# Performance work log

Measured on AMD Instinct MI355X. Metric: run time of the kernel, lower is better.

The kernel has to match this reference:

```python
import jax, jax.numpy as jnp
import numpy as np

V = 17  # number of skeleton joints (hard-coded in the torch module)
NUM_SUBSET = 3

def _dam_mask():
    # Reproduces the Python masking loops: zero block [12:17,12:17] and rows/cols {3,6,7,9,10}
    m = np.ones((V, V), np.float32)
    m[12:17, 12:17] = 0.0
    for j in (3, 6, 7, 9, 10):
        m[j, :] = 0.0
        m[:, j] = 0.0
    return jnp.asarray(m)

def setup_inputs() -> dict:
    key = jax.random.key(0)
    ks = jax.random.split(key, 8)
    N, Cin, Cout, T, G = 64, 64, 64, 256, 8
    return {
        "x": jax.random.normal(ks[0], (N, Cin, T, V), jnp.float32),
        "A_base": jax.random.uniform(ks[1], (NUM_SUBSET, V, V), jnp.float32),  # fixed adjacency buffer
        "DA": 0.01 * jax.random.normal(ks[2], (NUM_SUBSET, G, V, V), jnp.float32),   # DecoupleA param
        "DAM": 0.01 * jax.random.normal(ks[3], (NUM_SUBSET, G, V, V), jnp.float32),  # DecoupleAM param (masked, detached)
        "conv_w": jax.random.normal(ks[4], (NUM_SUBSET * Cout, Cin), jnp.float32) * (2.0 / Cin) ** 0.5,  # 1x1 conv
        "conv_b": jnp.zeros((NUM_SUBSET * Cout,), jnp.float32),
        "se_w": jax.random.normal(ks[5], (3,), jnp.float32) * 0.5,  # conv2_1: Conv1d(1,1,k=3,pad=1,no bias)
        "bn_gamma": jnp.full((Cout,), 1e-6, jnp.float32),  # bn_init(bn, 1e-6)
        "bn_beta": jnp.zeros((Cout,), jnp.float32),
    }

def reference(x, A_base, DA, DAM, conv_w, conv_b, se_w, bn_gamma, bn_beta):
    G = DA.shape[1]
    Cout = bn_gamma.shape[0]
    N, Cin, T, _ = x.shape
    # --- adjacency assembly: A (buffer, broadcast over groups) + DecoupleA + masked DecoupleAM ---
    A = A_base[:, None] + DA + DAM * _dam_mask()              # [3, G, V, V]
    # torch .repeat(1, out//groups, 1, 1) tiles along channel axis; + 0.04 from A_final loop
    A_final = jnp.tile(A, (1, Cout // G, 1, 1)) + 0.04        # [3, Cout, V, V]
    # --- 1x1 conv C_in -> 3*C_out ---
    m = jnp.einsum('nctv,kc->nktv', x, conv_w) + conv_b[None, :, None, None]
    m = m.reshape(N, NUM_SUBSET, Cout, T, V)
    # --- grouped adjacency aggregation (A_final has no batch dependence) ---
    m = jnp.einsum('nkctv,kcvw->nctw', m, A_final)            # [N, Cout, T, V]
    # --- SE-style channel attention: global avg pool -> Conv1d(k=3) over channels -> sigmoid gate ---
    p = m.mean(axis=(2, 3))                                   # [N, Cout]
    pp = jnp.pad(p, ((0, 0), (1, 1)))
    g = se_w[0] * pp[:, :-2] + se_w[1] * pp[:, 1:-1] + se_w[2] * pp[:, 2:]
    q = m + m * jax.nn.sigmoid(g)[:, :, None, None]
    # --- BatchNorm2d (training mode: batch stats over N,T,V) ---
    mu = q.mean(axis=(0, 2, 3), keepdims=True)
    var = q.var(axis=(0, 2, 3), keepdims=True)
    q = bn_gamma[None, :, None, None] * (q - mu) * jax.lax.rsqrt(var + 1e-5) + bn_beta[None, :, None, None]
    # --- residual (down == identity since in_channels == out_channels) and ReLU ---
    return jax.nn.relu(q + x)
```

## Files before the change

### kernel.cpp

```cpp
#include <hip/hip_runtime.h>
#include <math.h>

#define NN 64
#define CIN 64
#define COUT 64
#define TT 256
#define VV 17
#define NSUB 3
#define GG 8

#define WS_MB 0
#define WS_WBF 12288
#define WS_PSUM 18432
#define WS_SSQ 22528
#define WS_ACOEF 0
#define WS_BCOEF 4096

typedef short bh8 __attribute__((ext_vector_type(8)));
typedef float f32x4 __attribute__((ext_vector_type(4)));
typedef float f32x16 __attribute__((ext_vector_type(16)));
typedef unsigned short u16t;

__device__ __forceinline__ unsigned bf16r(float f) {
    unsigned u = __builtin_bit_cast(unsigned, f);
    return (u + 0x7fffu + ((u >> 16) & 1u)) >> 16;
}
__device__ __forceinline__ float bf2f(unsigned us) {
    return __builtin_bit_cast(float, us << 16);
}

__device__ __forceinline__ float mfull(const float* Ab, const float* DA, const float* DAM,
                                       int s, int g, int v, int w) {
    const unsigned bad = (1u << 3) | (1u << 6) | (1u << 7) | (1u << 9) | (1u << 10);
    float mask = ((v >= 12 && w >= 12) || ((bad >> v) & 1) || ((bad >> w) & 1)) ? 0.f : 1.f;
    int src = ((s * GG + g) * VV + v) * VV + w;
    return Ab[(s * VV + v) * VV + w] + DA[src] + DAM[src] * mask + 0.04f;
}

__global__ void gcn_prep(const float* __restrict__ Ab, const float* __restrict__ DA,
                         const float* __restrict__ DAM, const float* __restrict__ convw,
                         float* __restrict__ ws) {
    int t0 = blockIdx.x * 256 + threadIdx.x;
    int stride = gridDim.x * 256;
    u16t* wbf = (u16t*)(ws + WS_WBF);
    for (int i = t0; i < 192 * 64; i += stride) wbf[i] = (u16t)bf16r(convw[i]);
    u16t* mb = (u16t*)(ws + WS_MB);
    for (int i = t0; i < NSUB * GG * 32 * 32; i += stride) {
        int k = i & 31, w = (i >> 5) & 31, g = (i >> 10) & 7, s = i >> 13;
        u16t val = 0;
        if (w < VV && k < VV) val = (u16t)bf16r(mfull(Ab, DA, DAM, s, g, k, w));
        mb[i] = val;
    }
    for (int i = t0; i < 8192; i += stride) ws[WS_PSUM + i] = 0.f;
}

__global__ __launch_bounds__(512, 2) void gcn_pass1(const float* __restrict__ x,
                                                    const float* __restrict__ convb,
                                                    const float* __restrict__ ws,
                                                    float* __restrict__ out,
                                                    float* __restrict__ psum,
                                                    float* __restrict__ ssq) {
    __shared__ u16t xsT[272 * 72];
    __shared__ u16t Wl[192 * 72];
    __shared__ u16t mt[64 * 648];

    const int tid = threadIdx.x;
    const int wave = tid >> 6;
    const int l = tid & 63;
    const int c16 = l & 15;
    const int q4 = (l >> 4) & 3;
    const int c32 = l & 31;
    const int hi = l >> 5;
    const int n = blockIdx.x >> 2;

    const u16t* mbg = (const u16t*)(ws + WS_MB);
    const u16t* wbfg = (const u16t*)(ws + WS_WBF);

    for (int j = tid; j < 192 * 32; j += 512) {
        int row = j >> 5, c2 = j & 31;
        ((unsigned*)Wl)[row * 36 + c2] = ((const unsigned*)wbfg)[j];
    }
    for (int j = tid; j < (64 * 648) / 2; j += 512) ((unsigned*)mt)[j] = 0u;

    bh8 Badj[3], Badj2[3];
#pragma unroll
    for (int s = 0; s < 3; ++s) {
        const u16t* mrow = &mbg[((s * 8 + wave) * 32 + c32) * 32 + 8 * hi];
        Badj[s] = *(const bh8*)mrow;
        Badj2[s] = *(const bh8*)(mrow + 16);
    }
    const int cfs[3] = {wave, wave + 8, 16};

    float acc1[8], acc2[8];
#pragma unroll
    for (int j = 0; j < 8; ++j) { acc1[j] = 0.f; acc2[j] = 0.f; }

    __syncthreads();

    for (int k4 = 0; k4 < 4; ++k4) {
        const int tt = 4 * (blockIdx.x & 3) + k4;

        const float* xb = x + (size_t)n * 64 * 4352 + tt * 272;
#pragma unroll
        for (int k = 0; k < 4; ++k) {
            int cp = wave + 8 * k;
            const float* r0 = xb + (2 * cp) * 4352;
            const float* r1 = r0 + 4352;
#pragma unroll
            for (int cc = 0; cc < 5; ++cc) {
                int col = cc * 64 + l;
                if (col < 272) {
                    unsigned p = bf16r(r0[col]) | (bf16r(r1[col]) << 16);
                    ((unsigned*)xsT)[col * 36 + cp] = p;
                }
            }
        }
        __syncthreads();

        bh8 Bc[3][2];
#pragma unroll
        for (int cfi = 0; cfi < 3; ++cfi)
#pragma unroll
            for (int ks = 0; ks < 2; ++ks)
                Bc[cfi][ks] = *(const bh8*)&xsT[(16 * cfs[cfi] + c16) * 72 + 32 * ks + 8 * q4];

        f32x16 D2[4];
#pragma unroll
        for (int p = 0; p < 4; ++p) D2[p] = 0;

#pragma unroll
        for (int s = 0; s < 3; ++s) {
            f32x4 Dc[4][3];
#pragma unroll
            for (int rf = 0; rf < 4; ++rf) {
                f32x4 bias = *(const f32x4*)(convb + s * 64 + 16 * rf + 4 * q4);
#pragma unroll
                for (int cfi = 0; cfi < 3; ++cfi) Dc[rf][cfi] = bias;
            }
#pragma unroll
            for (int rf = 0; rf < 4; ++rf)
#pragma unroll
                for (int ks = 0; ks < 2; ++ks) {
                    bh8 A = *(const bh8*)&Wl[(s * 64 + 16 * rf + c16) * 72 + 32 * ks + 8 * q4];
                    Dc[rf][0] = __builtin_amdgcn_mfma_f32_16x16x32_bf16(A, Bc[0][ks], Dc[rf][0], 0, 0, 0);
                    Dc[rf][1] = __builtin_amdgcn_mfma_f32_16x16x32_bf16(A, Bc[1][ks], Dc[rf][1], 0, 0, 0);
                    if (wave == rf)
                        Dc[rf][2] = __builtin_amdgcn_mfma_f32_16x16x32_bf16(A, Bc[2][ks], Dc[rf][2], 0, 0, 0);
                }
            if (s > 0) __syncthreads();
#pragma unroll
            for (int rf = 0; rf < 4; ++rf)
#pragma unroll
                for (int cfi = 0; cfi < 3; ++cfi) {
                    if (cfi == 2 && wave != rf) continue;
                    int col = 16 * cfs[cfi] + c16;
                    int t = (col * 241) >> 12;
                    int v = col - 17 * t;
                    int base = (16 * rf + 4 * q4) * 648 + t * 40 + v;
#pragma unroll
                    for (int i = 0; i < 4; ++i)
                        mt[base + i * 648] = (u16t)bf16r(Dc[rf][cfi][i]);
                }
            __syncthreads();

#pragma unroll
            for (int p = 0; p < 4; ++p) {
                int coA = wave + 8 * (2 * p + (c32 >> 4));
                int base = coA * 648 + c16 * 40 + 8 * hi;
                bh8 a0 = *(const bh8*)&mt[base];
                bh8 a1 = *(const bh8*)&mt[base + 16];
                D2[p] = __builtin_amdgcn_mfma_f32_32x32x16_bf16(a0, Badj[s], D2[p], 0, 0, 0);
                D2[p] = __builtin_amdgcn_mfma_f32_32x32x16_bf16(a1, Badj2[s], D2[p], 0, 0, 0);
            }
        }

        u16t* stg = xsT;
#pragma unroll
        for (int p = 0; p < 4; ++p)
#pragma unroll
            for (int reg = 0; reg < 16; ++reg) {
                int row = (reg & 3) + 8 * (reg >> 2) + 4 * hi;
                int cosel = row >> 4;
                int t = row & 15;
                int co = wave + 8 * (2 * p + cosel);
                float val = D2[p][reg];
                if (c32 < 17) stg[co * 272 + t * 17 + c32] = (u16t)bf16r(val);
                if (cosel == 0) { acc1[2 * p] += val; acc2[2 * p] += val * val; }
                else            { acc1[2 * p + 1] += val; acc2[2 * p + 1] += val * val; }
            }
        __syncthreads();

        float* ob = out + ((size_t)n * 64) * 4352 + tt * 272;
#pragma unroll
        for (int it = 0; it < 9; ++it) {
            int c = tid + 512 * it;
            if (c < 4352) {
                int co = c / 68;
                int pos = (c - co * 68) * 4;
                uint2 u = *(const uint2*)&stg[co * 272 + pos];
                float4 v;
                v.x = bf2f(u.x & 0xffffu);
                v.y = bf2f(u.x >> 16);
                v.z = bf2f(u.y & 0xffffu);
                v.w = bf2f(u.y >> 16);
                *(float4*)(ob + co * 4352 + pos) = v;
            }
        }
        __syncthreads();
    }

#pragma unroll
    for (int j = 0; j < 8; ++j) {
        float s1 = acc1[j], s2 = acc2[j];
#pragma unroll
        for (int m = 1; m < 64; m <<= 1) {
            s1 += __shfl_xor(s1, m);
            s2 += __shfl_xor(s2, m);
        }
        if (l == 0) {
            atomicAdd(&psum[n * 64 + wave + 8 * j], s1);
            atomicAdd(&ssq[n * 64 + wave + 8 * j], s2);
        }
    }
}

__global__ void gcn_stats(const float* __restrict__ se_w, const float* __restrict__ gamma,
                          const float* __restrict__ beta, float* __restrict__ ws) {
    __shared__ float ps[4096], sc[4096], q2s[4096];
    __shared__ float mu_s[64], inv_s[64];
    int tid = threadIdx.x;
    const float* psum = ws + WS_PSUM;
    const float* ssq = ws + WS_SSQ;
    float* acoef = ws + WS_ACOEF;
    float* bcoef = ws + WS_BCOEF;
    for (int i = tid; i < 4096; i += 256) ps[i] = psum[i] * (1.f / (TT * VV));
    __syncthreads();
    float w0 = se_w[0], w1 = se_w[1], w2 = se_w[2];
    for (int i = tid; i < 4096; i += 256) {
        int c = i & 63;
        float pm = (c > 0) ? ps[i - 1] : 0.f;
        float pp = (c < 63) ? ps[i + 1] : 0.f;
        float gg = w0 * pm + w1 * ps[i] + w2 * pp;
        float s = 1.f + 1.f / (1.f + expf(-gg));
        sc[i] = s;
        q2s[i] = s * s * ssq[i];
    }
    __syncthreads();
    if (tid < 64) {
        float mu = 0.f, e2 = 0.f;
        for (int nn = 0; nn < 64; ++nn) {
            mu += sc[nn * 64 + tid] * ps[nn * 64 + tid];
            e2 += q2s[nn * 64 + tid];
        }
        mu *= (1.f / 64.f);
        e2 *= (1.f / (64.f * TT * VV));
        float var = e2 - mu * mu;
        mu_s[tid] = mu;
        inv_s[tid] = rsqrtf(var + 1e-5f);
    }
    __syncthreads();
    for (int i = tid; i < 4096; i += 256) {
        int c = i & 63;
        float gin = gamma[c] * inv_s[c];
        acoef[i] = gin * sc[i];
        bcoef[i] = beta[c] - gin * mu_s[c];
    }
}

__global__ __launch_bounds__(256) void gcn_final(const float* __restrict__ x,
                                                 const float* __restrict__ ws,
                                                 float* __restrict__ out) {
    const float* acoef = ws + WS_ACOEF;
    const float* bcoef = ws + WS_BCOEF;
    int i = blockIdx.x * 256 + threadIdx.x;
    const int total4 = (NN * COUT * TT * VV) / 4;
    if (i >= total4) return;
    int nc = i / ((TT * VV) / 4);
    float a = acoef[nc], b = bcoef[nc];
    float4 m = ((const float4*)out)[i];
    float4 xx = ((const float4*)x)[i];
    float4 r;
    r.x = fmaxf(fmaf(a, m.x, b) + xx.x, 0.f);
    r.y = fmaxf(fmaf(a, m.y, b) + xx.y, 0.f);
    r.z = fmaxf(fmaf(a, m.z, b) + xx.z, 0.f);
    r.w = fmaxf(fmaf(a, m.w, b) + xx.w, 0.f);
    ((float4*)out)[i] = r;
}

extern "C" void kernel_launch(void* const* d_in, const int* in_sizes, int n_in,
                              void* d_out, int out_size, void* d_ws, size_t ws_size,
                              hipStream_t stream) {
    const float* x = (const float*)d_in[0];
    const float* Ab = (const float*)d_in[1];
    const float* DA = (const float*)d_in[2];
    const float* DAM = (const float*)d_in[3];
    const float* convw = (const float*)d_in[4];
    const float* convb = (const float*)d_in[5];
    const float* sew = (const float*)d_in[6];
    const float* gamma = (const float*)d_in[7];
    const float* beta = (const float*)d_in[8];
    float* out = (float*)d_out;
    float* ws = (float*)d_ws;

    gcn_prep<<<16, 256, 0, stream>>>(Ab, DA, DAM, convw, ws);
    gcn_pass1<<<256, 512, 0, stream>>>(x, convb, ws, out, ws + WS_PSUM, ws + WS_SSQ);
    gcn_stats<<<1, 256, 0, stream>>>(sew, gamma, beta, ws);
    const int total4 = (NN * COUT * TT * VV) / 4;
    gcn_final<<<(total4 + 255) / 256, 256, 0, stream>>>(x, ws, out);
}
```

Before: 117.4 us.

## Halve pass1 tile size, store intermediate as bf16, raise occupancy

Pass1 now processes 8 time steps per tile (136 columns) with 512 blocks instead of 256, shrinks shared memory so four blocks can be resident per CU, and loads x as 8-channel packed vectors. When workspace is large enough, the intermediate pre-BN activation is written to a bf16 buffer in workspace instead of fp32 into the output, and a new final kernel reads it back. This halves the intermediate write and read traffic, and the extra workspace requirement is handled by falling back to the fp32 path.

```diff
diff --git a/kernel.cpp b/kernel.cpp
--- a/kernel.cpp
+++ b/kernel.cpp
@@ -15,6 +15,8 @@
 #define WS_SSQ 22528
 #define WS_ACOEF 0
 #define WS_BCOEF 4096
+#define M2BF_BYTE_OFF 131072ull
+#define M2BF_NEED (M2BF_BYTE_OFF + 2ull * 64 * 64 * 256 * 17)
 
 typedef short bh8 __attribute__((ext_vector_type(8)));
 typedef float f32x4 __attribute__((ext_vector_type(4)));
@@ -54,119 +56,131 @@
     for (int i = t0; i < 8192; i += stride) ws[WS_PSUM + i] = 0.f;
 }
 
-__global__ __launch_bounds__(512, 2) void gcn_pass1(const float* __restrict__ x,
+template <int BFOUT>
+__global__ __launch_bounds__(512, 4) void gcn_pass1(const float* __restrict__ x,
                                                     const float* __restrict__ convb,
                                                     const float* __restrict__ ws,
                                                     float* __restrict__ out,
+                                                    u16t* __restrict__ m2b,
                                                     float* __restrict__ psum,
                                                     float* __restrict__ ssq) {
-    __shared__ u16t xsT[272 * 72];
-    __shared__ u16t Wl[192 * 72];
-    __shared__ u16t mt[64 * 648];
+    __shared__ __align__(16) unsigned char smem[73984];
+    u16t* xsT = (u16t*)smem;
+    u16t* Wl = (u16t*)(smem + 20736);
+    u16t* mt = (u16t*)(smem + 48384);
 
     const int tid = threadIdx.x;
-    const int wave = tid >> 6;
+    const int wv = tid >> 6;
     const int l = tid & 63;
     const int c16 = l & 15;
     const int q4 = (l >> 4) & 3;
     const int c32 = l & 31;
     const int hi = l >> 5;
-    const int n = blockIdx.x >> 2;
-
-    const u16t* mbg = (const u16t*)(ws + WS_MB);
-    const u16t* wbfg = (const u16t*)(ws + WS_WBF);
-
-    for (int j = tid; j < 192 * 32; j += 512) {
-        int row = j >> 5, c2 = j & 31;
-        ((unsigned*)Wl)[row * 36 + c2] = ((const unsigned*)wbfg)[j];
-    }
-    for (int j = tid; j < (64 * 648) / 2; j += 512) ((unsigned*)mt)[j] = 0u;
-
+    const int n = blockIdx.x >> 3;
+
+    {
+        const unsigned* wsrc = (const unsigned*)(ws + WS_WBF);
+        unsigned* wd = (unsigned*)Wl;
+        for (int j = tid; j < 192 * 32; j += 512) wd[(j >> 5) * 36 + (j & 31)] = wsrc[j];
+        unsigned* mz = (unsigned*)mt;
+        for (int j = tid; j < 6400; j += 512) mz[j] = 0u;
+    }
+
+    const u16t* mb16 = (const u16t*)(ws + WS_MB);
     bh8 Badj[3], Badj2[3];
 #pragma unroll
     for (int s = 0; s < 3; ++s) {
-        const u16t* mrow = &mbg[((s * 8 + wave) * 32 + c32) * 32 + 8 * hi];
+        const u16t* mrow = &mb16[((s * 8 + wv) * 32 + c32) * 32 + 8 * hi];
         Badj[s] = *(const bh8*)mrow;
         Badj2[s] = *(const bh8*)(mrow + 16);
     }
-    const int cfs[3] = {wave, wave + 8, 16};
 
     float acc1[8], acc2[8];
 #pragma unroll
     for (int j = 0; j < 8; ++j) { acc1[j] = 0.f; acc2[j] = 0.f; }
 
-    __syncthreads();
-
     for (int k4 = 0; k4 < 4; ++k4) {
-        const int tt = 4 * (blockIdx.x & 3) + k4;
-
-        const float* xb = x + (size_t)n * 64 * 4352 + tt * 272;
-#pragma unroll
-        for (int k = 0; k < 4; ++k) {
-            int cp = wave + 8 * k;
-            const float* r0 = xb + (2 * cp) * 4352;
-            const float* r1 = r0 + 4352;
-#pragma unroll
-            for (int cc = 0; cc < 5; ++cc) {
-                int col = cc * 64 + l;
-                if (col < 272) {
-                    unsigned p = bf16r(r0[col]) | (bf16r(r1[col]) << 16);
-                    ((unsigned*)xsT)[col * 36 + cp] = p;
-                }
-            }
+        const int tt = (blockIdx.x & 7) * 4 + k4;
+
+        const float* xb = x + (size_t)n * 64 * 4352 + tt * 136;
+        for (int task = tid; task < 136 * 8; task += 512) {
+            int oct = task / 136;
+            int col = task - 136 * oct;
+            const float* src = xb + (8 * oct) * 4352 + col;
+            float r0 = src[0], r1 = src[4352], r2 = src[2 * 4352], r3 = src[3 * 4352];
+            float r4 = src[4 * 4352], r5 = src[5 * 4352], r6 = src[6 * 4352], r7 = src[7 * 4352];
+            uint4 pk;
+            pk.x = bf16r(r0) | (bf16r(r1) << 16);
+            pk.y = bf16r(r2) | (bf16r(r3) << 16);
+            pk.z = bf16r(r4) | (bf16r(r5) << 16);
+            pk.w = bf16r(r6) | (bf16r(r7) << 16);
+            *(uint4*)&((unsigned*)xsT)[col * 36 + oct * 4] = pk;
         }
         __syncthreads();
 
-        bh8 Bc[3][2];
-#pragma unroll
-        for (int cfi = 0; cfi < 3; ++cfi)
+        bh8 Bc[2], Bc8[2];
+#pragma unroll
+        for (int ks = 0; ks < 2; ++ks)
+            Bc[ks] = *(const bh8*)&xsT[(16 * wv + c16) * 72 + 32 * ks + 8 * q4];
+        if (wv < 4) {
 #pragma unroll
             for (int ks = 0; ks < 2; ++ks)
-                Bc[cfi][ks] = *(const bh8*)&xsT[(16 * cfs[cfi] + c16) * 72 + 32 * ks + 8 * q4];
-
-        f32x16 D2[4];
-#pragma unroll
-        for (int p = 0; p < 4; ++p) D2[p] = 0;
+                Bc8[ks] = *(const bh8*)&xsT[(128 + c16) * 72 + 32 * ks + 8 * q4];
+        }
+
+        f32x16 D2[2];
+        D2[0] = 0; D2[1] = 0;
 
 #pragma unroll
         for (int s = 0; s < 3; ++s) {
-            f32x4 Dc[4][3];
-#pragma unroll
-            for (int rf = 0; rf < 4; ++rf) {
-                f32x4 bias = *(const f32x4*)(convb + s * 64 + 16 * rf + 4 * q4);
-#pragma unroll
-                for (int cfi = 0; cfi < 3; ++cfi) Dc[rf][cfi] = bias;
-            }
+            f32x4 Dc[4], Dc8;
 #pragma unroll
             for (int rf = 0; rf < 4; ++rf)
+                Dc[rf] = *(const f32x4*)(convb + s * 64 + 16 * rf + 4 * q4);
+            if (wv < 4) Dc8 = *(const f32x4*)(convb + s * 64 + 16 * wv + 4 * q4);
+#pragma unroll
+            for (int ks = 0; ks < 2; ++ks)
+#pragma unroll
+                for (int rf = 0; rf < 4; ++rf) {
+                    bh8 A = *(const bh8*)&Wl[(s * 64 + 16 * rf + c16) * 72 + 32 * ks + 8 * q4];
+                    Dc[rf] = __builtin_amdgcn_mfma_f32_16x16x32_bf16(A, Bc[ks], Dc[rf], 0, 0, 0);
+                }
+            if (wv < 4) {
 #pragma unroll
                 for (int ks = 0; ks < 2; ++ks) {
-                    bh8 A = *(const bh8*)&Wl[(s * 64 + 16 * rf + c16) * 72 + 32 * ks + 8 * q4];
-                    Dc[rf][0] = __builtin_amdgcn_mfma_f32_16x16x32_bf16(A, Bc[0][ks], Dc[rf][0], 0, 0, 0);
-                    Dc[rf][1] = __builtin_amdgcn_mfma_f32_16x16x32_bf16(A, Bc[1][ks], Dc[rf][1], 0, 0, 0);
-                    if (wave == rf)
-                        Dc[rf][2] = __builtin_amdgcn_mfma_f32_16x16x32_bf16(A, Bc[2][ks], Dc[rf][2], 0, 0, 0);
-                }
+                    bh8 A = *(const bh8*)&Wl[(s * 64 + 16 * wv + c16) * 72 + 32 * ks + 8 * q4];
+                    Dc8 = __builtin_amdgcn_mfma_f32_16x16x32_bf16(A, Bc8[ks], Dc8, 0, 0, 0);
+                }
+            }
+
             if (s > 0) __syncthreads();
-#pragma unroll
-            for (int rf = 0; rf < 4; ++rf)
-#pragma unroll
-                for (int cfi = 0; cfi < 3; ++cfi) {
-                    if (cfi == 2 && wave != rf) continue;
-                    int col = 16 * cfs[cfi] + c16;
-                    int t = (col * 241) >> 12;
-                    int v = col - 17 * t;
-                    int base = (16 * rf + 4 * q4) * 648 + t * 40 + v;
+            {
+                int col = 16 * wv + c16;
+                int t = (col * 241) >> 12;
+                int v = col - 17 * t;
+                int off = t * 24 + v;
+#pragma unroll
+                for (int rf = 0; rf < 4; ++rf) {
+                    int co0 = 16 * rf + 4 * q4;
 #pragma unroll
                     for (int i = 0; i < 4; ++i)
-                        mt[base + i * 648] = (u16t)bf16r(Dc[rf][cfi][i]);
-                }
+                        mt[(co0 + i) * 200 + off] = (u16t)bf16r(Dc[rf][i]);
+                }
+                if (wv < 4 && c16 < 8) {
+                    int v8 = (128 + c16) - 119;
+                    int off8 = 7 * 24 + v8;
+                    int co0 = 16 * wv + 4 * q4;
+#pragma unroll
+                    for (int i = 0; i < 4; ++i)
+                        mt[(co0 + i) * 200 + off8] = (u16t)bf16r(Dc8[i]);
+                }
+            }
             __syncthreads();
 
 #pragma unroll
-            for (int p = 0; p < 4; ++p) {
-                int coA = wave + 8 * (2 * p + (c32 >> 4));
-                int base = coA * 648 + c16 * 40 + 8 * hi;
+            for (int p = 0; p < 2; ++p) {
+                int co = wv + 8 * ((c32 >> 3) + 4 * p);
+                int base = co * 200 + (c32 & 7) * 24 + 8 * hi;
                 bh8 a0 = *(const bh8*)&mt[base];
                 bh8 a1 = *(const bh8*)&mt[base + 16];
                 D2[p] = __builtin_amdgcn_mfma_f32_32x32x16_bf16(a0, Badj[s], D2[p], 0, 0, 0);
@@ -176,34 +190,48 @@
 
         u16t* stg = xsT;
 #pragma unroll
-        for (int p = 0; p < 4; ++p)
+        for (int p = 0; p < 2; ++p)
 #pragma unroll
             for (int reg = 0; reg < 16; ++reg) {
                 int row = (reg & 3) + 8 * (reg >> 2) + 4 * hi;
-                int cosel = row >> 4;
-                int t = row & 15;
-                int co = wave + 8 * (2 * p + cosel);
+                int cosel = row >> 3;
+                int t = row & 7;
+                int co = wv + 8 * (cosel + 4 * p);
                 float val = D2[p][reg];
-                if (c32 < 17) stg[co * 272 + t * 17 + c32] = (u16t)bf16r(val);
-                if (cosel == 0) { acc1[2 * p] += val; acc2[2 * p] += val * val; }
-                else            { acc1[2 * p + 1] += val; acc2[2 * p + 1] += val * val; }
+                if (c32 < 17) stg[co * 140 + t * 17 + c32] = (u16t)bf16r(val);
+                int j = cosel + 4 * p;
+                acc1[j] += val;
+                acc2[j] += val * val;
             }
         __syncthreads();
 
-        float* ob = out + ((size_t)n * 64) * 4352 + tt * 272;
-#pragma unroll
-        for (int it = 0; it < 9; ++it) {
-            int c = tid + 512 * it;
-            if (c < 4352) {
-                int co = c / 68;
-                int pos = (c - co * 68) * 4;
-                uint2 u = *(const uint2*)&stg[co * 272 + pos];
-                float4 v;
-                v.x = bf2f(u.x & 0xffffu);
-                v.y = bf2f(u.x >> 16);
-                v.z = bf2f(u.y & 0xffffu);
-                v.w = bf2f(u.y >> 16);
-                *(float4*)(ob + co * 4352 + pos) = v;
+        if (BFOUT) {
+            u16t* gm = m2b + (size_t)n * 64 * 4352 + tt * 136;
+#pragma unroll
+            for (int it = 0; it < 5; ++it) {
+                int c = tid + 512 * it;
+                if (c < 2176) {
+                    int co = c / 34;
+                    int pos = c - 34 * co;
+                    *(uint2*)(gm + co * 4352 + pos * 4) = *(const uint2*)&stg[co * 140 + pos * 4];
+                }
+            }
+        } else {
+            float* ob = out + (size_t)n * 64 * 4352 + tt * 136;
+#pragma unroll
+            for (int it = 0; it < 5; ++it) {
+                int c = tid + 512 * it;
+                if (c < 2176) {
+                    int co = c / 34;
+                    int pos = c - 34 * co;
+                    uint2 u = *(const uint2*)&stg[co * 140 + pos * 4];
+                    float4 v;
+                    v.x = bf2f(u.x & 0xffffu);
+                    v.y = bf2f(u.x >> 16);
+                    v.z = bf2f(u.y & 0xffffu);
+                    v.w = bf2f(u.y >> 16);
+                    *(float4*)(ob + co * 4352 + pos * 4) = v;
+                }
             }
         }
         __syncthreads();
@@ -218,8 +246,8 @@
             s2 += __shfl_xor(s2, m);
         }
         if (l == 0) {
-            atomicAdd(&psum[n * 64 + wave + 8 * j], s1);
-            atomicAdd(&ssq[n * 64 + wave + 8 * j], s2);
+            atomicAdd(&psum[n * 64 + wv + 8 * j], s1);
+            atomicAdd(&ssq[n * 64 + wv + 8 * j], s2);
         }
     }
 }
@@ -267,9 +295,9 @@
     }
 }
 
-__global__ __launch_bounds__(256) void gcn_final(const float* __restrict__ x,
-                                                 const float* __restrict__ ws,
-                                                 float* __restrict__ out) {
+__global__ __launch_bounds__(256) void gcn_final_f32(const float* __restrict__ x,
+                                                     const float* __restrict__ ws,
+                                                     float* __restrict__ out) {
     const float* acoef = ws + WS_ACOEF;
     const float* bcoef = ws + WS_BCOEF;
     int i = blockIdx.x * 256 + threadIdx.x;
@@ -287,6 +315,33 @@
     ((float4*)out)[i] = r;
 }
 
+__global__ __launch_bounds__(256) void gcn_final_bf16(const float* __restrict__ x,
+                                                      const float* __restrict__ ws,
+                                                      const u16t* __restrict__ m2b,
+                                                      float* __restrict__ out) {
+    const float* acoef = ws + WS_ACOEF;
+    const float* bcoef = ws + WS_BCOEF;
+    int i = blockIdx.x * 256 + threadIdx.x;
+    const int total8 = (NN * COUT * TT * VV) / 8;
+    if (i >= total8) return;
+    int nc = i / 544;
+    float a = acoef[nc], b = bcoef[nc];
+    uint4 u = *(const uint4*)(m2b + 8 * (size_t)i);
+    float4 x0 = ((const float4*)x)[2 * i];
+    float4 x1 = ((const float4*)x)[2 * i + 1];
+    float4 r0, r1;
+    r0.x = fmaxf(fmaf(a, bf2f(u.x & 0xffffu), b) + x0.x, 0.f);
+    r0.y = fmaxf(fmaf(a, bf2f(u.x >> 16), b) + x0.y, 0.f);
+    r0.z = fmaxf(fmaf(a, bf2f(u.y & 0xffffu), b) + x0.z, 0.f);
+    r0.w = fmaxf(fmaf(a, bf2f(u.y >> 16), b) + x0.w, 0.f);
+    r1.x = fmaxf(fmaf(a, bf2f(u.z & 0xffffu), b) + x1.x, 0.f);
+    r1.y = fmaxf(fmaf(a, bf2f(u.z >> 16), b) + x1.y, 0.f);
+    r1.z = fmaxf(fmaf(a, bf2f(u.w & 0xffffu), b) + x1.z, 0.f);
+    r1.w = fmaxf(fmaf(a, bf2f(u.w >> 16), b) + x1.w, 0.f);
+    ((float4*)out)[2 * i] = r0;
+    ((float4*)out)[2 * i + 1] = r1;
+}
+
 extern "C" void kernel_launch(void* const* d_in, const int* in_sizes, int n_in,
                               void* d_out, int out_size, void* d_ws, size_t ws_size,
                               hipStream_t stream) {
@@ -301,10 +356,21 @@
     const float* beta = (const float*)d_in[8];
     float* out = (float*)d_out;
     float* ws = (float*)d_ws;
+    u16t* m2b = (u16t*)((char*)d_ws + M2BF_BYTE_OFF);
+    const bool bfpath = ws_size >= M2BF_NEED;
 
     gcn_prep<<<16, 256, 0, stream>>>(Ab, DA, DAM, convw, ws);
-    gcn_pass1<<<256, 512, 0, stream>>>(x, convb, ws, out, ws + WS_PSUM, ws + WS_SSQ);
-    gcn_stats<<<1, 256, 0, stream>>>(sew, gamma, beta, ws);
-    const int total4 = (NN * COUT * TT * VV) / 4;
-    gcn_final<<<(total4 + 255) / 256, 256, 0, stream>>>(x, ws, out);
-}
+    if (bfpath) {
+        gcn_pass1<1><<<512, 512, 0, stream>>>(x, convb, ws, out, m2b,
+                                              ws + WS_PSUM, ws + WS_SSQ);
+        gcn_stats<<<1, 256, 0, stream>>>(sew, gamma, beta, ws);
+        const int total8 = (NN * COUT * TT * VV) / 8;
+        gcn_final_bf16<<<(total8 + 255) / 256, 256, 0, stream>>>(x, ws, m2b, out);
+    } else {
+        gcn_pass1<0><<<512, 512, 0, stream>>>(x, convb, ws, out, m2b,
+                                              ws + WS_PSUM, ws + WS_SSQ);
+        gcn_stats<<<1, 256, 0, stream>>>(sew, gamma, beta, ws);
+        const int total4 = (NN * COUT * TT * VV) / 4;
+        gcn_final_f32<<<(total4 + 255) / 256, 256, 0, stream>>>(x, ws, out);
+    }
+}
```

Measured after the change: 131.5 us, median of 2. 1.12x slower.
